# Kernel optimization log

Measured on AMD Instinct MI355X. Metric: run time of the kernel, lower is better.

Reference implementation:

```python
import jax, jax.numpy as jnp
import numpy as np

DIM = 192
H = W = 128
HEADS = 6
HEAD_DIM = DIM // HEADS
WIN = 8
SHIFT = 4
B = 16
LN_EPS = 1e-5


def setup_inputs() -> dict:
    key = jax.random.key(0)
    ks = jax.random.split(key, 16)
    d = DIM
    s = lambda *sh: 1.0 / np.sqrt(sh[-1])
    inp = {
        "x": jax.random.normal(ks[0], (B, H * W, d), jnp.float32),
        # torch Linear layout: (out, in)
        "qkv_w": jax.random.normal(ks[1], (3 * d, d), jnp.float32) * s(d, d),
        "qkv_b": jnp.zeros((3 * d,), jnp.float32),
        "proj_w": jax.random.normal(ks[2], (d, d), jnp.float32) * s(d, d),
        "proj_b": jnp.zeros((d,), jnp.float32),
        "n1_g": jnp.ones((d,), jnp.float32),
        "n1_b": jnp.zeros((d,), jnp.float32),
        "n2_g": jnp.ones((d,), jnp.float32),
        "n2_b": jnp.zeros((d,), jnp.float32),
        "w1": jax.random.normal(ks[3], (4 * d, d), jnp.float32) * s(d, d),
        "b1": jnp.zeros((4 * d,), jnp.float32),
        "w2": jax.random.normal(ks[4], (d, 4 * d), jnp.float32) * s(d, 4 * d),
        "b2": jnp.zeros((d,), jnp.float32),
    }
    return inp


def _ln(x, g, b):
    m = jnp.mean(x, -1, keepdims=True)
    v = jnp.mean(jnp.square(x - m), -1, keepdims=True)
    return (x - m) * jax.lax.rsqrt(v + LN_EPS) * g + b


def _l2norm(x):
    n = jnp.sqrt(jnp.sum(jnp.square(x), -1, keepdims=True))
    return x / jnp.maximum(n, 1e-12)


def _swin_forward(x, qkv_w, qkv_b, proj_w, proj_b, n1_g, n1_b, n2_g, n2_b, w1, b1, w2, b2):
    Bq, L, C = x.shape
    shortcut = x
    h = _ln(x, n1_g, n1_b).reshape(Bq, H, W, C)
    h = jnp.roll(h, (-SHIFT, -SHIFT), axis=(1, 2))
    nH, nW = H // WIN, W // WIN
    hw = h.reshape(Bq, nH, WIN, nW, WIN, C).transpose(0, 1, 3, 2, 4, 5)
    hw = hw.reshape(Bq * nH * nW, WIN * WIN, C)
    N = WIN * WIN
    qkv = hw @ qkv_w.T + qkv_b                      # (nWin, N, 3C)
    qkv = qkv.reshape(-1, N, 3, HEADS, HEAD_DIM).transpose(2, 0, 3, 1, 4)
    q, k, v = qkv[0], qkv[1], qkv[2]                # (nWin, heads, N, hd)
    q = _l2norm(q)
    k = _l2norm(k)
    scale = HEAD_DIM ** -0.5
    attn = jnp.einsum('whnd,whmd->whnm', q, k) * scale
    attn = attn - jnp.max(attn, -1, keepdims=True)
    attn = jax.nn.softmax(attn, -1)
    attn = jnp.clip(attn, 1e-6, 1.0)
    o = jnp.einsum('whnm,whmd->whnd', attn, v)      # (nWin, heads, N, hd)
    o = o.transpose(0, 2, 1, 3).reshape(-1, N, C)
    o = o @ proj_w.T + proj_b
    # window reverse
    o = o.reshape(Bq, nH, nW, WIN, WIN, C).transpose(0, 1, 3, 2, 4, 5)
    o = o.reshape(Bq, H, W, C)
    o = jnp.roll(o, (SHIFT, SHIFT), axis=(1, 2)).reshape(Bq, L, C)
    x = shortcut + o
    m = _ln(x, n2_g, n2_b)
    m = jax.nn.gelu(m @ w1.T + b1, approximate=False) @ w2.T + b2
    return x + m


def reference(x, qkv_w, qkv_b, proj_w, proj_b, n1_g, n1_b, n2_g, n2_b, w1, b1, w2, b2):
    return _swin_forward(x, qkv_w, qkv_b, proj_w, proj_b, n1_g, n1_b, n2_g, n2_b, w1, b1, w2, b2)
```

## Files before the change

kernel.cpp:

```cpp
#include <hip/hip_runtime.h>


typedef short s8v __attribute__((ext_vector_type(8)));
typedef float f4v __attribute__((ext_vector_type(4)));
typedef unsigned short u16;

static __device__ __forceinline__ float b2f(u16 u) {
    unsigned int x = ((unsigned int)u) << 16;
    return __builtin_bit_cast(float, x);
}
static __device__ __forceinline__ u16 f2b(float f) {
    unsigned int u = __builtin_bit_cast(unsigned int, f);
    u = (u + 0x7FFF + ((u >> 16) & 1)) >> 16;
    return (u16)u;
}
static __device__ __forceinline__ f4v mfma16(s8v a, s8v b, f4v c) {
    return __builtin_amdgcn_mfma_f32_16x16x32_bf16(a, b, c, 0, 0, 0);
}

static __device__ __forceinline__ float gelu_f(float v) {
    float z = v * 0.70710678118654752f;
    float az = fabsf(z);
    float t = 1.0f / (1.0f + 0.3275911f * az);
    float poly = t * (0.254829592f + t * (-0.284496736f + t * (1.421413741f
               + t * (-1.453152027f + t * 1.061405429f))));
    float erfv = 1.0f - poly * __expf(-az * az);
    erfv = __builtin_copysignf(erfv, z);
    return 0.5f * v * (1.0f + erfv);
}

#define SWZ(r, e) ((e) ^ (((r) & 7) << 3))

#define SZ_QKV  110592
#define SZ_PROJ  36864
#define SZ_W1   147456
#define SZ_W2   147456
#define OFF_PROJ (SZ_QKV)
#define OFF_W1   (SZ_QKV + SZ_PROJ)
#define OFF_W2   (SZ_QKV + SZ_PROJ + SZ_W1)
#define W_TOTAL  (SZ_QKV + SZ_PROJ + SZ_W1 + SZ_W2)

__global__ __launch_bounds__(256) void cvt_weights(
    const float* __restrict__ qkv_w, const float* __restrict__ proj_w,
    const float* __restrict__ w1, const float* __restrict__ w2,
    u16* __restrict__ dst)
{
    int i4 = (blockIdx.x * 256 + threadIdx.x) * 4;
    const float* src; int off;
    if (i4 < OFF_PROJ)     { src = qkv_w; off = i4; }
    else if (i4 < OFF_W1)  { src = proj_w; off = i4 - OFF_PROJ; }
    else if (i4 < OFF_W2)  { src = w1; off = i4 - OFF_W1; }
    else                   { src = w2; off = i4 - OFF_W2; }
    float4 v = *(const float4*)(src + off);
    ushort4 o;
    o.x = f2b(v.x); o.y = f2b(v.y); o.z = f2b(v.z); o.w = f2b(v.w);
    *(ushort4*)(dst + i4) = o;
}

__global__ __launch_bounds__(256, 3) void attn_fused(
    const float* __restrict__ x, const u16* __restrict__ Wqkv,
    const float* __restrict__ bqkv, const u16* __restrict__ Wproj,
    const float* __restrict__ bproj, const float* __restrict__ g1,
    const float* __restrict__ bn1, const float* __restrict__ g2,
    const float* __restrict__ bn2, u16* __restrict__ x2,
    u16* __restrict__ xln)
{
    __shared__ __align__(16) u16 lds[27136];
    u16* hs   = lds;
    u16* ks   = lds;
    u16* vt   = lds + 12288;
    u16* pscr = lds + 24576;

    const int tid = threadIdx.x;
    const int wv = tid >> 6, lane = tid & 63;
    const int lr = lane & 15, lq = lane >> 4;
    const int wloc = blockIdx.x;
    const int bb = wloc >> 8, wh = (wloc >> 4) & 15, ww = wloc & 15;
    u16* pw = pscr + wv * 640;

    {
        int tk = tid >> 2, q4 = tid & 3;
        int gh = (wh * 8 + (tk >> 3) + 4) & 127;
        int gw = (ww * 8 + (tk & 7) + 4) & 127;
        const float* xr = x + (((size_t)bb * 128 + gh) * 128 + gw) * 192 + q4 * 48;
        float4 xv[12];
        float s = 0.f, sq = 0.f;
#pragma unroll
        for (int i = 0; i < 12; i++) {
            xv[i] = *(const float4*)(xr + i * 4);
            s += xv[i].x + xv[i].y + xv[i].z + xv[i].w;
            sq += xv[i].x * xv[i].x + xv[i].y * xv[i].y
                + xv[i].z * xv[i].z + xv[i].w * xv[i].w;
        }
        s += __shfl_xor(s, 1); sq += __shfl_xor(sq, 1);
        s += __shfl_xor(s, 2); sq += __shfl_xor(sq, 2);
        float mean = s * (1.0f / 192.0f);
        float var = sq * (1.0f / 192.0f) - mean * mean;
        float rstd = 1.0f / sqrtf(var + 1e-5f);
#pragma unroll
        for (int i = 0; i < 12; i += 2) {
            int c0 = q4 * 48 + i * 4;
            float4 ga  = *(const float4*)(g1 + c0);
            float4 gb  = *(const float4*)(g1 + c0 + 4);
            float4 ba  = *(const float4*)(bn1 + c0);
            float4 bbv = *(const float4*)(bn1 + c0 + 4);
            s8v ov;
            ov[0] = (short)f2b((xv[i].x - mean) * rstd * ga.x + ba.x);
            ov[1] = (short)f2b((xv[i].y - mean) * rstd * ga.y + ba.y);
            ov[2] = (short)f2b((xv[i].z - mean) * rstd * ga.z + ba.z);
            ov[3] = (short)f2b((xv[i].w - mean) * rstd * ga.w + ba.w);
            ov[4] = (short)f2b((xv[i + 1].x - mean) * rstd * gb.x + bbv.x);
            ov[5] = (short)f2b((xv[i + 1].y - mean) * rstd * gb.y + bbv.y);
            ov[6] = (short)f2b((xv[i + 1].z - mean) * rstd * gb.z + bbv.z);
            ov[7] = (short)f2b((xv[i + 1].w - mean) * rstd * gb.w + bbv.w);
            *(s8v*)&hs[SWZ(tk, tk * 192 + c0)] = ov;
        }
    }
    __syncthreads();

    const int trow = 16 * wv + lr;
    s8v af[6];
#pragma unroll
    for (int k = 0; k < 6; k++)
        af[k] = *(const s8v*)&hs[SWZ(trow, trow * 192 + 32 * k + lq * 8)];
    __syncthreads();

    s8v aq[6];
#pragma unroll
    for (int h = 0; h < 6; h++) {
        f4v acc[6] = {};
#pragma unroll
        for (int k = 0; k < 6; k++) {
#pragma unroll
            for (int n = 0; n < 6; n++) {
                int wr = (n < 2) ? (32 * h + 16 * n + lr)
                       : (n < 4) ? (192 + 32 * h + 16 * (n - 2) + lr)
                                 : (384 + 32 * h + 16 * (n - 4) + lr);
                s8v bf = *(const s8v*)&Wqkv[(size_t)wr * 192 + 32 * k + lq * 8];
                acc[n] = mfma16(af[k], bf, acc[n]);
            }
        }
        float bq0 = bqkv[32 * h + lr],       bq1 = bqkv[32 * h + 16 + lr];
        float bk0 = bqkv[192 + 32 * h + lr], bk1 = bqkv[192 + 32 * h + 16 + lr];
        float bv0 = bqkv[384 + 32 * h + lr], bv1 = bqkv[384 + 32 * h + 16 + lr];
#pragma unroll
        for (int reg = 0; reg < 4; reg++) {
            int row = 16 * wv + lq * 4 + reg;
            float q0 = acc[0][reg] + bq0, q1 = acc[1][reg] + bq1;
            float ss = q0 * q0 + q1 * q1;
#pragma unroll
            for (int m = 1; m < 16; m <<= 1) ss += __shfl_xor(ss, m);
            float inv = 1.0f / fmaxf(sqrtf(ss), 1e-12f);
            pw[(lq * 4 + reg) * 40 + lr]      = f2b(q0 * inv);
            pw[(lq * 4 + reg) * 40 + 16 + lr] = f2b(q1 * inv);

            float k0v = acc[2][reg] + bk0, k1v = acc[3][reg] + bk1;
            ss = k0v * k0v + k1v * k1v;
#pragma unroll
            for (int m = 1; m < 16; m <<= 1) ss += __shfl_xor(ss, m);
            inv = 1.0f / fmaxf(sqrtf(ss), 1e-12f);
            ks[SWZ(row, row * 192 + 32 * h + lr)]      = f2b(k0v * inv);
            ks[SWZ(row, row * 192 + 32 * h + 16 + lr)] = f2b(k1v * inv);

            int d0 = 32 * h + lr, d1 = 32 * h + 16 + lr;
            vt[SWZ(d0, d0 * 64 + row)] = f2b(acc[4][reg] + bv0);
            vt[SWZ(d1, d1 * 64 + row)] = f2b(acc[5][reg] + bv1);
        }
        aq[h] = *(const s8v*)&pw[lr * 40 + lq * 8];
    }
    __syncthreads();

    f4v acc2[12] = {};
    const float scale = 0.17677669529663687f;
#pragma unroll
    for (int h = 0; h < 6; h++) {
        f4v accS[4] = {};
#pragma unroll
        for (int j = 0; j < 4; j++) {
            int kr = 16 * j + lr;
            s8v bk = *(const s8v*)&ks[SWZ(kr, kr * 192 + 32 * h + lq * 8)];
            accS[j] = mfma16(aq[h], bk, accS[j]);
        }
        float p[4][4];
#pragma unroll
        for (int reg = 0; reg < 4; reg++) {
            float v0 = accS[0][reg] * scale, v1 = accS[1][reg] * scale;
            float v2 = accS[2][reg] * scale, v3 = accS[3][reg] * scale;
            float mx = fmaxf(fmaxf(v0, v1), fmaxf(v2, v3));
#pragma unroll
            for (int m = 1; m < 16; m <<= 1) mx = fmaxf(mx, __shfl_xor(mx, m));
            float e0 = __expf(v0 - mx), e1 = __expf(v1 - mx);
            float e2 = __expf(v2 - mx), e3 = __expf(v3 - mx);
            float sum = e0 + e1 + e2 + e3;
#pragma unroll
            for (int m = 1; m < 16; m <<= 1) sum += __shfl_xor(sum, m);
            float is = 1.0f / sum;
            p[0][reg] = fminf(fmaxf(e0 * is, 1e-6f), 1.0f);
            p[1][reg] = fminf(fmaxf(e1 * is, 1e-6f), 1.0f);
            p[2][reg] = fminf(fmaxf(e2 * is, 1e-6f), 1.0f);
            p[3][reg] = fminf(fmaxf(e3 * is, 1e-6f), 1.0f);
        }
        f4v accO[2] = {};
#pragma unroll
        for (int reg = 0; reg < 4; reg++) {
            pw[(lq * 4 + reg) * 40 + lr]      = f2b(p[0][reg]);
            pw[(lq * 4 + reg) * 40 + 16 + lr] = f2b(p[1][reg]);
        }
        {
            s8v ap0 = *(const s8v*)&pw[lr * 40 + lq * 8];
#pragma unroll
            for (int n = 0; n < 2; n++) {
                int d = 32 * h + 16 * n + lr;
                s8v bvf = *(const s8v*)&vt[SWZ(d, d * 64 + lq * 8)];
                accO[n] = mfma16(ap0, bvf, accO[n]);
            }
        }
#pragma unroll
        for (int reg = 0; reg < 4; reg++) {
            pw[(lq * 4 + reg) * 40 + lr]      = f2b(p[2][reg]);
            pw[(lq * 4 + reg) * 40 + 16 + lr] = f2b(p[3][reg]);
        }
        {
            s8v ap1 = *(const s8v*)&pw[lr * 40 + lq * 8];
#pragma unroll
            for (int n = 0; n < 2; n++) {
                int d = 32 * h + 16 * n + lr;
                s8v bvf = *(const s8v*)&vt[SWZ(d, d * 64 + 32 + lq * 8)];
                accO[n] = mfma16(ap1, bvf, accO[n]);
            }
        }
#pragma unroll
        for (int n = 0; n < 2; n++)
#pragma unroll
            for (int reg = 0; reg < 4; reg++)
                pw[(lq * 4 + reg) * 40 + 16 * n + lr] = f2b(accO[n][reg]);
        s8v apj = *(const s8v*)&pw[lr * 40 + lq * 8];
#pragma unroll
        for (int n = 0; n < 12; n++) {
            s8v bpj = *(const s8v*)&Wproj[(size_t)(16 * n + lr) * 192 + 32 * h + lq * 8];
            acc2[n] = mfma16(apj, bpj, acc2[n]);
        }
    }

    float bpv[12], g2v[12], b2v[12];
#pragma unroll
    for (int n = 0; n < 12; n++) {
        int col = 16 * n + lr;
        bpv[n] = bproj[col]; g2v[n] = g2[col]; b2v[n] = bn2[col];
    }
#pragma unroll
    for (int reg = 0; reg < 4; reg++) {
        int tk = 16 * wv + lq * 4 + reg;
        int gh = (wh * 8 + (tk >> 3) + 4) & 127;
        int gw = (ww * 8 + (tk & 7) + 4) & 127;
        size_t base = (((size_t)bb * 128 + gh) * 128 + gw) * 192;
        float vv[12];
        float s = 0.f, sq = 0.f;
#pragma unroll
        for (int n = 0; n < 12; n++) {
            float v = acc2[n][reg] + bpv[n] + x[base + 16 * n + lr];
            vv[n] = v; s += v; sq += v * v;
        }
        s += __shfl_xor(s, 1); sq += __shfl_xor(sq, 1);
        s += __shfl_xor(s, 2); sq += __shfl_xor(sq, 2);
        s += __shfl_xor(s, 4); sq += __shfl_xor(sq, 4);
        s += __shfl_xor(s, 8); sq += __shfl_xor(sq, 8);
        float mean = s * (1.0f / 192.0f);
        float var = sq * (1.0f / 192.0f) - mean * mean;
        float rstd = 1.0f / sqrtf(var + 1e-5f);
#pragma unroll
        for (int n = 0; n < 12; n++) {
            size_t idx = base + 16 * n + lr;
            x2[idx]  = f2b(vv[n]);
            xln[idx] = f2b((vv[n] - mean) * rstd * g2v[n] + b2v[n]);
        }
    }
}

__global__ __launch_bounds__(256) void gemm_gelu(
    const u16* __restrict__ A,
    const u16* __restrict__ W,
    const float* __restrict__ B1,
    u16* __restrict__ C)
{
    __shared__ __align__(16) u16 As[128 * 40];
    __shared__ __align__(16) u16 Bs[128 * 40];
    const int tid = threadIdx.x;
    const int wv = tid >> 6, lane = tid & 63;
    const int lr = lane & 15, lq = lane >> 4;
    const int wm = (wv >> 1) * 64, wn = (wv & 1) * 64;
    const size_t m0 = (size_t)blockIdx.y * 128;
    const int n0 = blockIdx.x * 128;

    const int ar = tid >> 1, ac = (tid & 1) * 16;
    const u16* aptr = A + (m0 + ar) * 192 + ac;
    const u16* bptr = W + (size_t)(n0 + ar) * 192 + ac;

    f4v acc[4][4] = {};
    for (int k0 = 0; k0 < 192; k0 += 32) {
        __syncthreads();
        *(s8v*)&As[ar * 40 + ac]     = *(const s8v*)(aptr + k0);
        *(s8v*)&As[ar * 40 + ac + 8] = *(const s8v*)(aptr + k0 + 8);
        *(s8v*)&Bs[ar * 40 + ac]     = *(const s8v*)(bptr + k0);
        *(s8v*)&Bs[ar * 40 + ac + 8] = *(const s8v*)(bptr + k0 + 8);
        __syncthreads();
        s8v af[4], bf[4];
#pragma unroll
        for (int mt = 0; mt < 4; mt++)
            af[mt] = *(const s8v*)&As[(wm + 16 * mt + lr) * 40 + lq * 8];
#pragma unroll
        for (int nt = 0; nt < 4; nt++)
            bf[nt] = *(const s8v*)&Bs[(wn + 16 * nt + lr) * 40 + lq * 8];
#pragma unroll
        for (int mt = 0; mt < 4; mt++)
#pragma unroll
            for (int nt = 0; nt < 4; nt++)
                acc[mt][nt] = mfma16(af[mt], bf[nt], acc[mt][nt]);
    }

#pragma unroll
    for (int nt = 0; nt < 4; nt++) {
        int col = n0 + wn + 16 * nt + lr;
        float bb = B1[col];
#pragma unroll
        for (int mt = 0; mt < 4; mt++)
#pragma unroll
            for (int reg = 0; reg < 4; reg++) {
                size_t row = m0 + wm + 16 * mt + lq * 4 + reg;
                C[row * 768 + col] = f2b(gelu_f(acc[mt][nt][reg] + bb));
            }
    }
}

__global__ __launch_bounds__(256) void gemm_out(
    const u16* __restrict__ A,
    const u16* __restrict__ W,
    const float* __restrict__ B2,
    const u16* __restrict__ resid,
    float* __restrict__ Cout)
{
    __shared__ __align__(16) u16 As[256 * 40];
    __shared__ __align__(16) u16 Bs[64 * 40];
    const int tid = threadIdx.x;
    const int wv = tid >> 6, lane = tid & 63;
    const int lr = lane & 15, lq = lane >> 4;
    const int wm = wv * 64;
    const size_t m0 = (size_t)blockIdx.y * 256;
    const int n0 = blockIdx.x * 64;

    const u16* aptr = A + (m0 + tid) * 768;
    const int br = tid >> 2, bc = (tid & 3) * 8;
    const u16* bptr = W + (size_t)(n0 + br) * 768 + bc;

    f4v acc[4][4] = {};
    for (int k0 = 0; k0 < 768; k0 += 32) {
        __syncthreads();
#pragma unroll
        for (int i = 0; i < 4; i++)
            *(s8v*)&As[tid * 40 + i * 8] = *(const s8v*)(aptr + k0 + i * 8);
        *(s8v*)&Bs[br * 40 + bc] = *(const s8v*)(bptr + k0);
        __syncthreads();
        s8v af[4], bf[4];
#pragma unroll
        for (int mt = 0; mt < 4; mt++)
            af[mt] = *(const s8v*)&As[(wm + 16 * mt + lr) * 40 + lq * 8];
#pragma unroll
        for (int nt = 0; nt < 4; nt++)
            bf[nt] = *(const s8v*)&Bs[(16 * nt + lr) * 40 + lq * 8];
#pragma unroll
        for (int mt = 0; mt < 4; mt++)
#pragma unroll
            for (int nt = 0; nt < 4; nt++)
                acc[mt][nt] = mfma16(af[mt], bf[nt], acc[mt][nt]);
    }

#pragma unroll
    for (int nt = 0; nt < 4; nt++) {
        int col = n0 + 16 * nt + lr;
        float bb = B2[col];
#pragma unroll
        for (int mt = 0; mt < 4; mt++)
#pragma unroll
            for (int reg = 0; reg < 4; reg++) {
                size_t row = m0 + wm + 16 * mt + lq * 4 + reg;
                Cout[row * 192 + col] = acc[mt][nt][reg] + bb
                                      + b2f(resid[row * 192 + col]);
            }
    }
}

extern "C" void kernel_launch(void* const* d_in, const int* in_sizes, int n_in,
                              void* d_out, int out_size, void* d_ws, size_t ws_size,
                              hipStream_t stream) {
    const float* x      = (const float*)d_in[0];
    const float* qkv_w  = (const float*)d_in[1];
    const float* qkv_b  = (const float*)d_in[2];
    const float* proj_w = (const float*)d_in[3];
    const float* proj_b = (const float*)d_in[4];
    const float* n1_g   = (const float*)d_in[5];
    const float* n1_b   = (const float*)d_in[6];
    const float* n2_g   = (const float*)d_in[7];
    const float* n2_b   = (const float*)d_in[8];
    const float* w1     = (const float*)d_in[9];
    const float* b1     = (const float*)d_in[10];
    const float* w2     = (const float*)d_in[11];
    const float* b2     = (const float*)d_in[12];
    float* out = (float*)d_out;

    u16* wsu = (u16*)d_ws;
    u16* wQ  = wsu;
    u16* wP  = wsu + OFF_PROJ;
    u16* wW1 = wsu + OFF_W1;
    u16* wW2 = wsu + OFF_W2;
    char* dataBase = (char*)d_ws + (1 << 20);
    size_t avail = (ws_size > (1 << 20)) ? ws_size - (1 << 20) : 0;

    dim3 blk(256);
    cvt_weights<<<W_TOTAL / 1024, blk, 0, stream>>>(qkv_w, proj_w, w1, w2, wsu);

    const size_t perTok = (size_t)(192 + 192 + 768) * 2;
    int Bs = 4;
    while (Bs > 1 && (size_t)Bs * 16384 * perTok > avail) Bs >>= 1;
    const int nslice = 16 / Bs;
    const size_t stok = (size_t)Bs * 16384;
    u16* x2buf  = (u16*)dataBase;
    u16* xlnbuf = x2buf + stok * 192;
    u16* mhbuf  = xlnbuf + stok * 192;

    for (int s = 0; s < nslice; s++) {
        const float* xs = x + (size_t)s * stok * 192;
        float* outs = out + (size_t)s * stok * 192;
        attn_fused<<<Bs * 256, blk, 0, stream>>>(xs, wQ, qkv_b, wP, proj_b,
                                                 n1_g, n1_b, n2_g, n2_b,
                                                 x2buf, xlnbuf);
        gemm_gelu<<<dim3(6, Bs * 128), blk, 0, stream>>>(xlnbuf, wW1, b1, mhbuf);
        gemm_out<<<dim3(3, Bs * 64), blk, 0, stream>>>(mhbuf, wW2, b2,
                                                       x2buf, outs);
    }
}
```

Measured before the change: 1.532 ms.

## Per-head attention LDS staging and direct global-to-LDS loads in MLP GEMMs

The attention kernel now computes QKV, attention and projection one head at a time, storing only that head's K and V in LDS. This shrinks LDS use enough to raise the occupancy hint from 3 to 4 blocks. The two MLP GEMMs switch from register-staged tile copies to buffer loads that write straight into LDS, using an XOR-swizzled unpadded layout. The cost is two barriers per head, the A fragments being re-read from LDS for every head, and a dependence on the global_load_lds builtin's lane-to-address mapping.

After: 1.478 ms. -3.5%, faster.

```diff
diff --git a/kernel.cpp b/kernel.cpp
--- a/kernel.cpp
+++ b/kernel.cpp
@@ -16,6 +16,12 @@
 }
 static __device__ __forceinline__ f4v mfma16(s8v a, s8v b, f4v c) {
     return __builtin_amdgcn_mfma_f32_16x16x32_bf16(a, b, c, 0, 0, 0);
+}
+
+static __device__ __forceinline__ void gload16(const u16* g, u16* l) {
+    __builtin_amdgcn_global_load_lds(
+        (const __attribute__((address_space(1))) unsigned int*)g,
+        (__attribute__((address_space(3))) unsigned int*)l, 16, 0, 0);
 }
 
 static __device__ __forceinline__ float gelu_f(float v) {
@@ -57,7 +63,127 @@
     *(ushort4*)(dst + i4) = o;
 }
 
-__global__ __launch_bounds__(256, 3) void attn_fused(
+static __device__ __forceinline__ void qkv_head(
+    int h, const u16* hs, const u16* __restrict__ Wqkv,
+    const float* __restrict__ bqkv, u16* kb, u16* vb, u16* pw,
+    s8v& aqOut, int wv, int lr, int lq)
+{
+    const int trow = 16 * wv + lr;
+    f4v acc[6] = {};
+#pragma unroll
+    for (int k = 0; k < 6; k++) {
+        s8v af = *(const s8v*)&hs[SWZ(trow, trow * 192 + 32 * k + lq * 8)];
+#pragma unroll
+        for (int n = 0; n < 6; n++) {
+            int wr = (n < 2) ? (32 * h + 16 * n + lr)
+                   : (n < 4) ? (192 + 32 * h + 16 * (n - 2) + lr)
+                             : (384 + 32 * h + 16 * (n - 4) + lr);
+            s8v bf = *(const s8v*)&Wqkv[(size_t)wr * 192 + 32 * k + lq * 8];
+            acc[n] = mfma16(af, bf, acc[n]);
+        }
+    }
+    float bq0 = bqkv[32 * h + lr],       bq1 = bqkv[32 * h + 16 + lr];
+    float bk0 = bqkv[192 + 32 * h + lr], bk1 = bqkv[192 + 32 * h + 16 + lr];
+    float bv0 = bqkv[384 + 32 * h + lr], bv1 = bqkv[384 + 32 * h + 16 + lr];
+#pragma unroll
+    for (int reg = 0; reg < 4; reg++) {
+        int row = 16 * wv + lq * 4 + reg;
+        float q0 = acc[0][reg] + bq0, q1 = acc[1][reg] + bq1;
+        float ss = q0 * q0 + q1 * q1;
+#pragma unroll
+        for (int m = 1; m < 16; m <<= 1) ss += __shfl_xor(ss, m);
+        float inv = 1.0f / fmaxf(sqrtf(ss), 1e-12f);
+        pw[(lq * 4 + reg) * 40 + lr]      = f2b(q0 * inv);
+        pw[(lq * 4 + reg) * 40 + 16 + lr] = f2b(q1 * inv);
+
+        float k0v = acc[2][reg] + bk0, k1v = acc[3][reg] + bk1;
+        ss = k0v * k0v + k1v * k1v;
+#pragma unroll
+        for (int m = 1; m < 16; m <<= 1) ss += __shfl_xor(ss, m);
+        inv = 1.0f / fmaxf(sqrtf(ss), 1e-12f);
+        kb[SWZ(row, row * 32 + lr)]      = f2b(k0v * inv);
+        kb[SWZ(row, row * 32 + 16 + lr)] = f2b(k1v * inv);
+
+        vb[SWZ(lr, lr * 64 + row)]             = f2b(acc[4][reg] + bv0);
+        vb[SWZ(16 + lr, (16 + lr) * 64 + row)] = f2b(acc[5][reg] + bv1);
+    }
+    aqOut = *(const s8v*)&pw[lr * 40 + lq * 8];
+}
+
+static __device__ __forceinline__ void attn_head(
+    int h, s8v aq, const u16* kb, const u16* vb, u16* pw,
+    f4v* acc2, const u16* __restrict__ Wproj, int wv, int lr, int lq)
+{
+    f4v accS[4] = {};
+#pragma unroll
+    for (int j = 0; j < 4; j++) {
+        int kr = 16 * j + lr;
+        s8v bk = *(const s8v*)&kb[SWZ(kr, kr * 32 + lq * 8)];
+        accS[j] = mfma16(aq, bk, accS[j]);
+    }
+    const float scale = 0.17677669529663687f;
+    float p[4][4];
+#pragma unroll
+    for (int reg = 0; reg < 4; reg++) {
+        float v0 = accS[0][reg] * scale, v1 = accS[1][reg] * scale;
+        float v2 = accS[2][reg] * scale, v3 = accS[3][reg] * scale;
+        float mx = fmaxf(fmaxf(v0, v1), fmaxf(v2, v3));
+#pragma unroll
+        for (int m = 1; m < 16; m <<= 1) mx = fmaxf(mx, __shfl_xor(mx, m));
+        float e0 = __expf(v0 - mx), e1 = __expf(v1 - mx);
+        float e2 = __expf(v2 - mx), e3 = __expf(v3 - mx);
+        float sum = e0 + e1 + e2 + e3;
+#pragma unroll
+        for (int m = 1; m < 16; m <<= 1) sum += __shfl_xor(sum, m);
+        float is = 1.0f / sum;
+        p[0][reg] = fminf(fmaxf(e0 * is, 1e-6f), 1.0f);
+        p[1][reg] = fminf(fmaxf(e1 * is, 1e-6f), 1.0f);
+        p[2][reg] = fminf(fmaxf(e2 * is, 1e-6f), 1.0f);
+        p[3][reg] = fminf(fmaxf(e3 * is, 1e-6f), 1.0f);
+    }
+    f4v accO[2] = {};
+#pragma unroll
+    for (int reg = 0; reg < 4; reg++) {
+        pw[(lq * 4 + reg) * 40 + lr]      = f2b(p[0][reg]);
+        pw[(lq * 4 + reg) * 40 + 16 + lr] = f2b(p[1][reg]);
+    }
+    {
+        s8v ap = *(const s8v*)&pw[lr * 40 + lq * 8];
+#pragma unroll
+        for (int n = 0; n < 2; n++) {
+            int d = 16 * n + lr;
+            s8v bvf = *(const s8v*)&vb[SWZ(d, d * 64 + lq * 8)];
+            accO[n] = mfma16(ap, bvf, accO[n]);
+        }
+    }
+#pragma unroll
+    for (int reg = 0; reg < 4; reg++) {
+        pw[(lq * 4 + reg) * 40 + lr]      = f2b(p[2][reg]);
+        pw[(lq * 4 + reg) * 40 + 16 + lr] = f2b(p[3][reg]);
+    }
+    {
+        s8v ap = *(const s8v*)&pw[lr * 40 + lq * 8];
+#pragma unroll
+        for (int n = 0; n < 2; n++) {
+            int d = 16 * n + lr;
+            s8v bvf = *(const s8v*)&vb[SWZ(d, d * 64 + 32 + lq * 8)];
+            accO[n] = mfma16(ap, bvf, accO[n]);
+        }
+    }
+#pragma unroll
+    for (int n = 0; n < 2; n++)
+#pragma unroll
+        for (int reg = 0; reg < 4; reg++)
+            pw[(lq * 4 + reg) * 40 + 16 * n + lr] = f2b(accO[n][reg]);
+    s8v apj = *(const s8v*)&pw[lr * 40 + lq * 8];
+#pragma unroll
+    for (int n = 0; n < 12; n++) {
+        s8v bpj = *(const s8v*)&Wproj[(size_t)(16 * n + lr) * 192 + 32 * h + lq * 8];
+        acc2[n] = mfma16(apj, bpj, acc2[n]);
+    }
+}
+
+__global__ __launch_bounds__(256, 4) void attn_fused(
     const float* __restrict__ x, const u16* __restrict__ Wqkv,
     const float* __restrict__ bqkv, const u16* __restrict__ Wproj,
     const float* __restrict__ bproj, const float* __restrict__ g1,
@@ -65,11 +191,11 @@
     const float* __restrict__ bn2, u16* __restrict__ x2,
     u16* __restrict__ xln)
 {
-    __shared__ __align__(16) u16 lds[27136];
-    u16* hs   = lds;
-    u16* ks   = lds;
-    u16* vt   = lds + 12288;
-    u16* pscr = lds + 24576;
+    __shared__ __align__(16) u16 lds[18944];
+    u16* hs = lds;
+    u16* kb = lds + 12288;
+    u16* vb = lds + 14336;
+    u16* pscr = lds + 16384;
 
     const int tid = threadIdx.x;
     const int wv = tid >> 6, lane = tid & 63;
@@ -116,130 +242,15 @@
             *(s8v*)&hs[SWZ(tk, tk * 192 + c0)] = ov;
         }
     }
-    __syncthreads();
-
-    const int trow = 16 * wv + lr;
-    s8v af[6];
-#pragma unroll
-    for (int k = 0; k < 6; k++)
-        af[k] = *(const s8v*)&hs[SWZ(trow, trow * 192 + 32 * k + lq * 8)];
-    __syncthreads();
-
-    s8v aq[6];
-#pragma unroll
+
+    f4v acc2[12] = {};
+#pragma unroll 1
     for (int h = 0; h < 6; h++) {
-        f4v acc[6] = {};
-#pragma unroll
-        for (int k = 0; k < 6; k++) {
-#pragma unroll
-            for (int n = 0; n < 6; n++) {
-                int wr = (n < 2) ? (32 * h + 16 * n + lr)
-                       : (n < 4) ? (192 + 32 * h + 16 * (n - 2) + lr)
-                                 : (384 + 32 * h + 16 * (n - 4) + lr);
-                s8v bf = *(const s8v*)&Wqkv[(size_t)wr * 192 + 32 * k + lq * 8];
-                acc[n] = mfma16(af[k], bf, acc[n]);
-            }
-        }
-        float bq0 = bqkv[32 * h + lr],       bq1 = bqkv[32 * h + 16 + lr];
-        float bk0 = bqkv[192 + 32 * h + lr], bk1 = bqkv[192 + 32 * h + 16 + lr];
-        float bv0 = bqkv[384 + 32 * h + lr], bv1 = bqkv[384 + 32 * h + 16 + lr];
-#pragma unroll
-        for (int reg = 0; reg < 4; reg++) {
-            int row = 16 * wv + lq * 4 + reg;
-            float q0 = acc[0][reg] + bq0, q1 = acc[1][reg] + bq1;
-            float ss = q0 * q0 + q1 * q1;
-#pragma unroll
-            for (int m = 1; m < 16; m <<= 1) ss += __shfl_xor(ss, m);
-            float inv = 1.0f / fmaxf(sqrtf(ss), 1e-12f);
-            pw[(lq * 4 + reg) * 40 + lr]      = f2b(q0 * inv);
-            pw[(lq * 4 + reg) * 40 + 16 + lr] = f2b(q1 * inv);
-
-            float k0v = acc[2][reg] + bk0, k1v = acc[3][reg] + bk1;
-            ss = k0v * k0v + k1v * k1v;
-#pragma unroll
-            for (int m = 1; m < 16; m <<= 1) ss += __shfl_xor(ss, m);
-            inv = 1.0f / fmaxf(sqrtf(ss), 1e-12f);
-            ks[SWZ(row, row * 192 + 32 * h + lr)]      = f2b(k0v * inv);
-            ks[SWZ(row, row * 192 + 32 * h + 16 + lr)] = f2b(k1v * inv);
-
-            int d0 = 32 * h + lr, d1 = 32 * h + 16 + lr;
-            vt[SWZ(d0, d0 * 64 + row)] = f2b(acc[4][reg] + bv0);
-            vt[SWZ(d1, d1 * 64 + row)] = f2b(acc[5][reg] + bv1);
-        }
-        aq[h] = *(const s8v*)&pw[lr * 40 + lq * 8];
-    }
-    __syncthreads();
-
-    f4v acc2[12] = {};
-    const float scale = 0.17677669529663687f;
-#pragma unroll
-    for (int h = 0; h < 6; h++) {
-        f4v accS[4] = {};
-#pragma unroll
-        for (int j = 0; j < 4; j++) {
-            int kr = 16 * j + lr;
-            s8v bk = *(const s8v*)&ks[SWZ(kr, kr * 192 + 32 * h + lq * 8)];
-            accS[j] = mfma16(aq[h], bk, accS[j]);
-        }
-        float p[4][4];
-#pragma unroll
-        for (int reg = 0; reg < 4; reg++) {
-            float v0 = accS[0][reg] * scale, v1 = accS[1][reg] * scale;
-            float v2 = accS[2][reg] * scale, v3 = accS[3][reg] * scale;
-            float mx = fmaxf(fmaxf(v0, v1), fmaxf(v2, v3));
-#pragma unroll
-            for (int m = 1; m < 16; m <<= 1) mx = fmaxf(mx, __shfl_xor(mx, m));
-            float e0 = __expf(v0 - mx), e1 = __expf(v1 - mx);
-            float e2 = __expf(v2 - mx), e3 = __expf(v3 - mx);
-            float sum = e0 + e1 + e2 + e3;
-#pragma unroll
-            for (int m = 1; m < 16; m <<= 1) sum += __shfl_xor(sum, m);
-            float is = 1.0f / sum;
-            p[0][reg] = fminf(fmaxf(e0 * is, 1e-6f), 1.0f);
-            p[1][reg] = fminf(fmaxf(e1 * is, 1e-6f), 1.0f);
-            p[2][reg] = fminf(fmaxf(e2 * is, 1e-6f), 1.0f);
-            p[3][reg] = fminf(fmaxf(e3 * is, 1e-6f), 1.0f);
-        }
-        f4v accO[2] = {};
-#pragma unroll
-        for (int reg = 0; reg < 4; reg++) {
-            pw[(lq * 4 + reg) * 40 + lr]      = f2b(p[0][reg]);
-            pw[(lq * 4 + reg) * 40 + 16 + lr] = f2b(p[1][reg]);
-        }
-        {
-            s8v ap0 = *(const s8v*)&pw[lr * 40 + lq * 8];
-#pragma unroll
-            for (int n = 0; n < 2; n++) {
-                int d = 32 * h + 16 * n + lr;
-                s8v bvf = *(const s8v*)&vt[SWZ(d, d * 64 + lq * 8)];
-                accO[n] = mfma16(ap0, bvf, accO[n]);
-            }
-        }
-#pragma unroll
-        for (int reg = 0; reg < 4; reg++) {
-            pw[(lq * 4 + reg) * 40 + lr]      = f2b(p[2][reg]);
-            pw[(lq * 4 + reg) * 40 + 16 + lr] = f2b(p[3][reg]);
-        }
-        {
-            s8v ap1 = *(const s8v*)&pw[lr * 40 + lq * 8];
-#pragma unroll
-            for (int n = 0; n < 2; n++) {
-                int d = 32 * h + 16 * n + lr;
-                s8v bvf = *(const s8v*)&vt[SWZ(d, d * 64 + 32 + lq * 8)];
-                accO[n] = mfma16(ap1, bvf, accO[n]);
-            }
-        }
-#pragma unroll
-        for (int n = 0; n < 2; n++)
-#pragma unroll
-            for (int reg = 0; reg < 4; reg++)
-                pw[(lq * 4 + reg) * 40 + 16 * n + lr] = f2b(accO[n][reg]);
-        s8v apj = *(const s8v*)&pw[lr * 40 + lq * 8];
-#pragma unroll
-        for (int n = 0; n < 12; n++) {
-            s8v bpj = *(const s8v*)&Wproj[(size_t)(16 * n + lr) * 192 + 32 * h + lq * 8];
-            acc2[n] = mfma16(apj, bpj, acc2[n]);
-        }
+        s8v aq;
+        qkv_head(h, hs, Wqkv, bqkv, kb, vb, pw, aq, wv, lr, lq);
+        __syncthreads();
+        attn_head(h, aq, kb, vb, pw, acc2, Wproj, wv, lr, lq);
+        __syncthreads();
     }
 
     float bpv[12], g2v[12], b2v[12];
@@ -283,8 +294,8 @@
     const float* __restrict__ B1,
     u16* __restrict__ C)
 {
-    __shared__ __align__(16) u16 As[128 * 40];
-    __shared__ __align__(16) u16 Bs[128 * 40];
+    __shared__ __align__(16) u16 As[128 * 32];
+    __shared__ __align__(16) u16 Bs[128 * 32];
     const int tid = threadIdx.x;
     const int wv = tid >> 6, lane = tid & 63;
     const int lr = lane & 15, lq = lane >> 4;
@@ -292,25 +303,30 @@
     const size_t m0 = (size_t)blockIdx.y * 128;
     const int n0 = blockIdx.x * 128;
 
-    const int ar = tid >> 1, ac = (tid & 1) * 16;
-    const u16* aptr = A + (m0 + ar) * 192 + ac;
-    const u16* bptr = W + (size_t)(n0 + ar) * 192 + ac;
+    const int srow = lane >> 2;
+    const int sc8 = (((lane & 3) ^ (srow & 3)) << 3);
+    const u16* aptr = A + (m0 + 32 * wv + srow) * 192 + sc8;
+    const u16* bptr = W + (size_t)(n0 + 32 * wv + srow) * 192 + sc8;
 
     f4v acc[4][4] = {};
     for (int k0 = 0; k0 < 192; k0 += 32) {
         __syncthreads();
-        *(s8v*)&As[ar * 40 + ac]     = *(const s8v*)(aptr + k0);
-        *(s8v*)&As[ar * 40 + ac + 8] = *(const s8v*)(aptr + k0 + 8);
-        *(s8v*)&Bs[ar * 40 + ac]     = *(const s8v*)(bptr + k0);
-        *(s8v*)&Bs[ar * 40 + ac + 8] = *(const s8v*)(bptr + k0 + 8);
+        gload16(aptr + k0,            &As[(32 * wv) * 32]);
+        gload16(aptr + 16 * 192 + k0, &As[(32 * wv + 16) * 32]);
+        gload16(bptr + k0,            &Bs[(32 * wv) * 32]);
+        gload16(bptr + 16 * 192 + k0, &Bs[(32 * wv + 16) * 32]);
         __syncthreads();
         s8v af[4], bf[4];
 #pragma unroll
-        for (int mt = 0; mt < 4; mt++)
-            af[mt] = *(const s8v*)&As[(wm + 16 * mt + lr) * 40 + lq * 8];
-#pragma unroll
-        for (int nt = 0; nt < 4; nt++)
-            bf[nt] = *(const s8v*)&Bs[(wn + 16 * nt + lr) * 40 + lq * 8];
+        for (int mt = 0; mt < 4; mt++) {
+            int r = wm + 16 * mt + lr;
+            af[mt] = *(const s8v*)&As[r * 32 + ((lq ^ (r & 3)) << 3)];
+        }
+#pragma unroll
+        for (int nt = 0; nt < 4; nt++) {
+            int r = wn + 16 * nt + lr;
+            bf[nt] = *(const s8v*)&Bs[r * 32 + ((lq ^ (r & 3)) << 3)];
+        }
 #pragma unroll
         for (int mt = 0; mt < 4; mt++)
 #pragma unroll
@@ -339,8 +355,8 @@
     const u16* __restrict__ resid,
     float* __restrict__ Cout)
 {
-    __shared__ __align__(16) u16 As[256 * 40];
-    __shared__ __align__(16) u16 Bs[64 * 40];
+    __shared__ __align__(16) u16 As[256 * 32];
+    __shared__ __align__(16) u16 Bs[64 * 32];
     const int tid = threadIdx.x;
     const int wv = tid >> 6, lane = tid & 63;
     const int lr = lane & 15, lq = lane >> 4;
@@ -348,25 +364,31 @@
     const size_t m0 = (size_t)blockIdx.y * 256;
     const int n0 = blockIdx.x * 64;
 
-    const u16* aptr = A + (m0 + tid) * 768;
-    const int br = tid >> 2, bc = (tid & 3) * 8;
-    const u16* bptr = W + (size_t)(n0 + br) * 768 + bc;
+    const int srow = lane >> 2;
+    const int sc8 = (((lane & 3) ^ (srow & 3)) << 3);
+    const u16* aptr = A + (m0 + 64 * wv + srow) * 768 + sc8;
+    const u16* bptr = W + (size_t)(n0 + 16 * wv + srow) * 768 + sc8;
 
     f4v acc[4][4] = {};
     for (int k0 = 0; k0 < 768; k0 += 32) {
         __syncthreads();
 #pragma unroll
-        for (int i = 0; i < 4; i++)
-            *(s8v*)&As[tid * 40 + i * 8] = *(const s8v*)(aptr + k0 + i * 8);
-        *(s8v*)&Bs[br * 40 + bc] = *(const s8v*)(bptr + k0);
+        for (int j = 0; j < 4; j++)
+            gload16(aptr + (size_t)(16 * j) * 768 + k0,
+                    &As[(64 * wv + 16 * j) * 32]);
+        gload16(bptr + k0, &Bs[(16 * wv) * 32]);
         __syncthreads();
         s8v af[4], bf[4];
 #pragma unroll
-        for (int mt = 0; mt < 4; mt++)
-            af[mt] = *(const s8v*)&As[(wm + 16 * mt + lr) * 40 + lq * 8];
-#pragma unroll
-        for (int nt = 0; nt < 4; nt++)
-            bf[nt] = *(const s8v*)&Bs[(16 * nt + lr) * 40 + lq * 8];
+        for (int mt = 0; mt < 4; mt++) {
+            int r = wm + 16 * mt + lr;
+            af[mt] = *(const s8v*)&As[r * 32 + ((lq ^ (r & 3)) << 3)];
+        }
+#pragma unroll
+        for (int nt = 0; nt < 4; nt++) {
+            int r = 16 * nt + lr;
+            bf[nt] = *(const s8v*)&Bs[r * 32 + ((lq ^ (r & 3)) << 3)];
+        }
 #pragma unroll
         for (int mt = 0; mt < 4; mt++)
 #pragma unroll
```
